# Optimization experiments

Measured on AMD Instinct MI355X. Metric: run time of the kernel, lower is better.

Reference implementation:

```python
import jax, jax.numpy as jnp
import numpy as np

EMBED = 256
HEADS = 8
LEVELS = 4
POINTS = 4
HD = EMBED // HEADS  # 32
SHAPES = np.array([[100, 100], [50, 50], [25, 25], [13, 13]], dtype=np.int64)  # (H_l, W_l)


def setup_inputs() -> dict:
    key = jax.random.key(0)
    ks = jax.random.split(key, 12)
    nv = int(SHAPES.prod(-1).sum())  # 13294
    bs, nq, d = 2, nv, EMBED
    level_start = np.concatenate([[0], SHAPES.prod(-1).cumsum()[:-1]])
    s = 0.02
    return {
        "query": jax.random.normal(ks[0], (bs, nq, d), jnp.float32),
        "reference_points": jax.random.uniform(ks[1], (bs, nq, LEVELS, 2), jnp.float32),
        "value": jax.random.normal(ks[2], (bs, nv, d), jnp.float32),
        "spatial_shapes": jnp.asarray(SHAPES, jnp.int32),
        "level_start_index": jnp.asarray(level_start, jnp.int32),
        "key_padding_mask": jnp.zeros((bs, nv), jnp.bool_),
        "W_samp": jax.random.normal(ks[3], (HEADS * LEVELS * POINTS * 2, d), jnp.float32) * s,
        "b_samp": jax.random.normal(ks[4], (HEADS * LEVELS * POINTS * 2,), jnp.float32),
        "W_attn": jax.random.normal(ks[5], (HEADS * LEVELS * POINTS, d), jnp.float32) * s,
        "b_attn": jnp.zeros((HEADS * LEVELS * POINTS,), jnp.float32),
        "W_val": jax.random.normal(ks[6], (d, d), jnp.float32) * s,
        "b_val": jnp.zeros((d,), jnp.float32),
        "W_out": jax.random.normal(ks[7], (d, d), jnp.float32) * s,
        "b_out": jnp.zeros((d,), jnp.float32),
    }


def _msda_core(value_bhnd, shapes_np, starts_np, loc, attn):
    """value_bhnd: (bs, H, nv, hd); loc: (bs, nq, H, L, P, 2) in [0,1]; attn: (bs, nq, H, L, P)."""
    bs, heads, nv, hd = value_bhnd.shape
    nq = loc.shape[1]
    out = jnp.zeros((bs, nq, heads, hd), value_bhnd.dtype)
    for l in range(LEVELS):
        H, W = int(shapes_np[l, 0]), int(shapes_np[l, 1])
        start = int(starts_np[l])
        v = jax.lax.dynamic_slice_in_dim(value_bhnd, start, H * W, axis=2)  # (bs, heads, H*W, hd)
        # grid_sample(align_corners=False): pixel coord = loc * size - 0.5
        lx = loc[:, :, :, l, :, 0] * W - 0.5  # (bs, nq, heads, P)
        ly = loc[:, :, :, l, :, 1] * H - 0.5
        x0 = jnp.floor(lx)
        y0 = jnp.floor(ly)
        tx = lx - x0
        ty = ly - y0
        x0i = x0.astype(jnp.int32)
        y0i = y0.astype(jnp.int32)
        samp = jnp.zeros((bs, heads, nq, POINTS, hd), value_bhnd.dtype)
        for dy, wy in ((0, 1.0 - ty), (1, ty)):
            for dx, wx in ((0, 1.0 - tx), (1, tx)):
                xi = x0i + dx
                yi = y0i + dy
                valid = (xi >= 0) & (xi < W) & (yi >= 0) & (yi < H)  # zeros padding
                idx = jnp.clip(yi, 0, H - 1) * W + jnp.clip(xi, 0, W - 1)  # (bs, nq, heads, P)
                idx_t = idx.transpose(0, 2, 1, 3).reshape(bs, heads, nq * POINTS)
                g = jnp.take_along_axis(v, idx_t[..., None], axis=2)
                g = g.reshape(bs, heads, nq, POINTS, hd)
                w = jnp.where(valid, wx * wy, 0.0).transpose(0, 2, 1, 3)[..., None]
                samp = samp + g * w
        out = out + jnp.einsum("bhqpd,bqhp->bqhd", samp, attn[:, :, :, l, :])
    return out.reshape(bs, nq, heads * hd)


def reference(query, reference_points, value, spatial_shapes, level_start_index,
              key_padding_mask, W_samp, b_samp, W_attn, b_attn, W_val, b_val, W_out, b_out):
    bs, nq, d = query.shape
    v = value @ W_val.T + b_val
    v = jnp.where(key_padding_mask[..., None], 0.0, v)
    v = v.reshape(bs, -1, HEADS, HD).transpose(0, 2, 1, 3)  # (bs, heads, nv, hd)
    off = (query @ W_samp.T + b_samp).reshape(bs, nq, HEADS, LEVELS, POINTS, 2)
    attn = (query @ W_attn.T + b_attn).reshape(bs, nq, HEADS, LEVELS * POINTS)
    attn = jax.nn.softmax(attn, axis=-1).reshape(bs, nq, HEADS, LEVELS, POINTS)
    ss = np.asarray(spatial_shapes)
    starts = np.asarray(level_start_index)
    # offset normalizer is (W, H) per level
    norm = jnp.asarray(ss[:, ::-1].copy(), jnp.float32)
    loc = reference_points[:, :, None, :, None, :] + off / norm[None, None, None, :, None, :]
    out = _msda_core(v, ss, starts, loc, attn)
    return out @ W_out.T + b_out
```

## Files before the change

kernel.cpp:

```cpp
#include <hip/hip_runtime.h>
#include <hip/hip_bf16.h>
#include <hip/hip_fp16.h>
#include <cstdint>
#include <cstddef>

#define EMBED  256
#define NV_PER_B 13294
#define M_PAD   26624
#define NQPB   8

__constant__ const int c_H[4]  = {100, 50, 25, 13};
__constant__ const int c_W[4]  = {100, 50, 25, 13};
__constant__ const int c_ST[4] = {0, 10000, 12500, 13125};

typedef __attribute__((ext_vector_type(8))) short bf16x8;
typedef __attribute__((ext_vector_type(4))) float f32x4;

__device__ inline short f2bf(float x) {
    __hip_bfloat16 h = __float2bfloat16(x);
    return *reinterpret_cast<short*>(&h);
}

__global__ __launch_bounds__(256) void convert_kernel(
    const float* __restrict__ q,  const float* __restrict__ v,
    const float* __restrict__ wv, const float* __restrict__ wsamp,
    const float* __restrict__ wattn, const float* __restrict__ wo,
    const float* __restrict__ bsamp, const float* __restrict__ battn,
    short* __restrict__ q_bf, short* __restrict__ v_bf,
    short* __restrict__ wv_bf, short* __restrict__ wcat_bf,
    short* __restrict__ wo_bf, float* __restrict__ bias_cat,
    int n_real4, int n_pad4)
{
    const int i = blockIdx.x * 256 + threadIdx.x;
    if (i < n_pad4) {
        float4 a = make_float4(0.f, 0.f, 0.f, 0.f);
        float4 b = make_float4(0.f, 0.f, 0.f, 0.f);
        if (i < n_real4) {
            a = ((const float4*)q)[i];
            b = ((const float4*)v)[i];
        }
        ((short4*)q_bf)[i] = make_short4(f2bf(a.x), f2bf(a.y), f2bf(a.z), f2bf(a.w));
        ((short4*)v_bf)[i] = make_short4(f2bf(b.x), f2bf(b.y), f2bf(b.z), f2bf(b.w));
    }
    if (i < 16384) {
        float4 a = ((const float4*)wv)[i];
        float4 c = ((const float4*)wo)[i];
        ((short4*)wv_bf)[i] = make_short4(f2bf(a.x), f2bf(a.y), f2bf(a.z), f2bf(a.w));
        ((short4*)wo_bf)[i] = make_short4(f2bf(c.x), f2bf(c.y), f2bf(c.z), f2bf(c.w));
    }
    if (i < 24576) {
        float4 a = (i < 16384) ? ((const float4*)wsamp)[i]
                               : ((const float4*)wattn)[i - 16384];
        ((short4*)wcat_bf)[i] = make_short4(f2bf(a.x), f2bf(a.y), f2bf(a.z), f2bf(a.w));
    }
    if (i < 96) {
        float4 a = (i < 64) ? ((const float4*)bsamp)[i]
                            : ((const float4*)battn)[i - 64];
        ((float4*)bias_cat)[i] = a;
    }
}

__device__ __forceinline__ void gemm_kloop(
    const short* __restrict__ A, const short* __restrict__ Wt,
    int bm, int bn, char* smem, f32x4 (&acc)[4][4],
    int t, int wave, int lane)
{
    constexpr int K = 256;
    const int row0 = t >> 2, row1 = row0 + 64;
    const int kbl  = t & 3;
    const int kbg0 = kbl ^ (row0 & 3);
    const int kbg1 = kbl ^ (row1 & 3);
    const size_t a0 = (size_t)(bm + row0) * K + kbg0 * 8;
    const size_t a1 = (size_t)(bm + row1) * K + kbg1 * 8;
    const size_t b0 = (size_t)(bn + row0) * K + kbg0 * 8;
    const size_t b1 = (size_t)(bn + row1) * K + kbg1 * 8;
    const int lr16 = lane & 15, qk = lane >> 4;
    const int swz  = (qk ^ (lr16 & 3)) * 16;
    const int wrow = wave & 1, wcol = wave >> 1;

    auto issue = [&](int stage, int k0) {
        char* sa = smem + stage * 16384 + wave * 1024;
        char* sb = sa + 8192;
        __builtin_amdgcn_global_load_lds(
            (const __attribute__((address_space(1))) void*)(A + a0 + k0),
            (__attribute__((address_space(3))) void*)(sa), 16, 0, 0);
        __builtin_amdgcn_global_load_lds(
            (const __attribute__((address_space(1))) void*)(A + a1 + k0),
            (__attribute__((address_space(3))) void*)(sa + 4096), 16, 0, 0);
        __builtin_amdgcn_global_load_lds(
            (const __attribute__((address_space(1))) void*)(Wt + b0 + k0),
            (__attribute__((address_space(3))) void*)(sb), 16, 0, 0);
        __builtin_amdgcn_global_load_lds(
            (const __attribute__((address_space(1))) void*)(Wt + b1 + k0),
            (__attribute__((address_space(3))) void*)(sb + 4096), 16, 0, 0);
    };

    issue(0, 0);
    #pragma unroll
    for (int it = 0; it < 8; ++it) {
        __syncthreads();
        if (it + 1 < 8) issue((it + 1) & 1, (it + 1) * 32);
        const char* sa = smem + (it & 1) * 16384;
        const char* sb = sa + 8192;
        bf16x8 af[4], bfr[4];
        #pragma unroll
        for (int mi = 0; mi < 4; ++mi)
            af[mi] = *(const bf16x8*)(sa + (wrow * 64 + mi * 16 + lr16) * 64 + swz);
        #pragma unroll
        for (int ni = 0; ni < 4; ++ni)
            bfr[ni] = *(const bf16x8*)(sb + (wcol * 64 + ni * 16 + lr16) * 64 + swz);
        #pragma unroll
        for (int mi = 0; mi < 4; ++mi)
            #pragma unroll
            for (int ni = 0; ni < 4; ++ni)
                acc[mi][ni] = __builtin_amdgcn_mfma_f32_16x16x32_bf16(
                    af[mi], bfr[ni], acc[mi][ni], 0, 0, 0);
    }
}

__global__ __launch_bounds__(256) void gemm_mega_kernel(
    const short* __restrict__ v_bf, const short* __restrict__ wv_bf,
    const float* __restrict__ b_val, __half* __restrict__ vproj,
    const short* __restrict__ q_bf, const short* __restrict__ wcat_bf,
    const float* __restrict__ bias_cat, __half* __restrict__ qo)
{
    __shared__ __align__(16) char smem[36864];
    const int t = threadIdx.x;
    const int wave = t >> 6, lane = t & 63;
    const int lr16 = lane & 15, qk = lane >> 4;
    const int wrow = wave & 1, wcol = wave >> 1;
    const int y = blockIdx.y;
    const int bm = blockIdx.x * 128;

    const short* A; const short* Wt; const float* bias; __half* Cc; int Nst, bn;
    if (y < 2) { A = v_bf; Wt = wv_bf;   bias = b_val;    Cc = vproj; Nst = 256; bn = y * 128; }
    else       { A = q_bf; Wt = wcat_bf; bias = bias_cat; Cc = qo;    Nst = 384; bn = (y - 2) * 128; }

    f32x4 acc[4][4] = {};
    gemm_kloop(A, Wt, bm, bn, smem, acc, t, wave, lane);

    __syncthreads();
    __half* ep = (__half*)(smem + wave * 9216);
    const int colbase = bn + wcol * 64;
    float bv[4];
    #pragma unroll
    for (int ni = 0; ni < 4; ++ni) bv[ni] = bias[colbase + ni * 16 + lr16];
    #pragma unroll
    for (int mi = 0; mi < 4; ++mi)
        #pragma unroll
        for (int ni = 0; ni < 4; ++ni)
            #pragma unroll
            for (int r = 0; r < 4; ++r)
                ep[(mi * 16 + qk * 4 + r) * 72 + ni * 16 + lr16] =
                    __float2half(acc[mi][ni][r] + bv[ni]);
    __syncthreads();
    const int er = lane >> 3, ec = (lane & 7) * 8;
    #pragma unroll
    for (int pass = 0; pass < 8; ++pass) {
        const int r = pass * 8 + er;
        const int4 vv = *(const int4*)&ep[r * 72 + ec];
        const int grow = bm + wrow * 64 + r;
        *(int4*)&Cc[(size_t)grow * Nst + colbase + ec] = vv;
    }
}

__global__ __launch_bounds__(256) void gemm_out_kernel(
    const short* __restrict__ corebf, const short* __restrict__ wo_bf,
    const float* __restrict__ b_out, float* __restrict__ C, int M)
{
    __shared__ __align__(16) char smem[36864];
    const int t = threadIdx.x;
    const int wave = t >> 6, lane = t & 63;
    const int lr16 = lane & 15, qk = lane >> 4;
    const int wrow = wave & 1, wcol = wave >> 1;
    const int bm = blockIdx.x * 128, bn = blockIdx.y * 128;

    f32x4 acc[4][4] = {};
    gemm_kloop(corebf, wo_bf, bm, bn, smem, acc, t, wave, lane);

    const int colbase = bn + wcol * 64;
    float bv[4];
    #pragma unroll
    for (int ni = 0; ni < 4; ++ni) bv[ni] = b_out[colbase + ni * 16 + lr16];
    float* ep = (float*)(smem + wave * 8704);
    #pragma unroll
    for (int p = 0; p < 2; ++p) {
        __syncthreads();
        #pragma unroll
        for (int mh = 0; mh < 2; ++mh) {
            const int mi = p * 2 + mh;
            #pragma unroll
            for (int ni = 0; ni < 4; ++ni)
                #pragma unroll
                for (int r = 0; r < 4; ++r)
                    ep[(mh * 16 + qk * 4 + r) * 68 + ni * 16 + lr16] =
                        acc[mi][ni][r] + bv[ni];
        }
        __syncthreads();
        const int er = lane >> 4, ec = (lane & 15) * 4;
        #pragma unroll
        for (int j = 0; j < 8; ++j) {
            const int r = j * 4 + er;
            const float4 vv = *(const float4*)&ep[r * 68 + ec];
            const int grow = bm + wrow * 64 + p * 32 + r;
            if (grow < M)
                *(float4*)&C[(size_t)grow * 256 + colbase + ec] = vv;
        }
    }
}

__global__ __launch_bounds__(256) void msda_core_kernel(
    const __half* __restrict__ vproj,
    const float* __restrict__ refp,
    const __half* __restrict__ qo,
    short* __restrict__ core,
    int nq, int nv, int M)
{
    const int bq0 = blockIdx.x * NQPB;
    const int t = threadIdx.x;

    __shared__ float s_w[NQPB * 128];
    __shared__ float s_ref[NQPB * 8];
    __shared__ unsigned int s_tap[NQPB * 8][65];

    #pragma unroll
    for (int i = 0; i < 4; ++i) {
        const int s = t + i * 256;
        const int q = s >> 7, r = s & 127;
        s_w[s] = __half2float(qo[(size_t)(bq0 + q) * 384 + 256 + r]);
    }
    if (t < NQPB * 8) {
        const int gq = min(bq0 + (t >> 3), M - 1);
        s_ref[t] = refp[(size_t)gq * 8 + (t & 7)];
    }
    __syncthreads();

    if (t < NQPB * 8) {
        const int base = (t >> 3) * 128 + (t & 7) * 16;
        float m = -1e30f;
        #pragma unroll
        for (int j = 0; j < 16; ++j) m = fmaxf(m, s_w[base + j]);
        float e[16]; float ssum = 0.f;
        #pragma unroll
        for (int j = 0; j < 16; ++j) { e[j] = expf(s_w[base + j] - m); ssum += e[j]; }
        const float inv = 1.f / ssum;
        #pragma unroll
        for (int j = 0; j < 16; ++j) s_w[base + j] = e[j] * inv;
    }
    __syncthreads();

    #pragma unroll
    for (int i = 0; i < 4; ++i) {
        const int s = t + i * 256;
        const int q = s >> 7, r = s & 127;
        const int h = r >> 4, lp = r & 15, l = lp >> 2;
        const int gq = bq0 + q;
        const float2 off = __half22float2(*(const __half2*)&qo[(size_t)gq * 384 + r * 2]);
        const float rx = s_ref[q * 8 + l * 2];
        const float ry = s_ref[q * 8 + l * 2 + 1];
        const int W = c_W[l], H = c_H[l], st = c_ST[l];
        const float fW = (float)W, fH = (float)H;
        const float lx = (rx + off.x / fW) * fW - 0.5f;
        const float ly = (ry + off.y / fH) * fH - 0.5f;
        const float x0f = floorf(lx), y0f = floorf(ly);
        const float fx = lx - x0f, fy = ly - y0f;
        const int x0 = (int)x0f, y0 = (int)y0f;
        const float aw = s_w[s];
        const float wx[2] = {1.f - fx, fx};
        const float wy[2] = {1.f - fy, fy};
        #pragma unroll
        for (int dy = 0; dy < 2; ++dy) {
            #pragma unroll
            for (int dx = 0; dx < 2; ++dx) {
                const int xi = x0 + dx, yi = y0 + dy;
                const bool ok = (xi >= 0) & (xi < W) & (yi >= 0) & (yi < H);
                const unsigned int idx = ok ? (unsigned int)(st + yi * W + xi) : 0u;
                const float w = ok ? aw * wy[dy] * wx[dx] : 0.f;
                const unsigned int pw = (unsigned int)__half_as_ushort(__float2half(w));
                s_tap[q * 8 + h][lp * 4 + dy * 2 + dx] = idx | (pw << 16);
            }
        }
    }
    __syncthreads();

    const int q   = t >> 5;
    const int l32 = t & 31;
    const int h   = l32 >> 2;
    const int c8  = l32 & 3;
    const int gq  = bq0 + q;
    const int b   = (gq >= nq) ? 1 : 0;
    const __half* __restrict__ vb = vproj + (size_t)b * nv * EMBED + h * 32 + c8 * 8;
    const unsigned int* __restrict__ taps = s_tap[q * 8 + h];

    float a[8] = {0.f, 0.f, 0.f, 0.f, 0.f, 0.f, 0.f, 0.f};
    #pragma unroll 8
    for (int j = 0; j < 64; ++j) {
        const unsigned int u = taps[j];
        const float w = __half2float(__ushort_as_half((unsigned short)(u >> 16)));
        const int4 raw = *(const int4*)(vb + (size_t)(u & 0xFFFFu) * EMBED);
        const __half2* hh = (const __half2*)&raw;
        float2 f;
        f = __half22float2(hh[0]); a[0] = fmaf(w, f.x, a[0]); a[1] = fmaf(w, f.y, a[1]);
        f = __half22float2(hh[1]); a[2] = fmaf(w, f.x, a[2]); a[3] = fmaf(w, f.y, a[3]);
        f = __half22float2(hh[2]); a[4] = fmaf(w, f.x, a[4]); a[5] = fmaf(w, f.y, a[5]);
        f = __half22float2(hh[3]); a[6] = fmaf(w, f.x, a[6]); a[7] = fmaf(w, f.y, a[7]);
    }

    if (gq < M) {
        __align__(16) short o[8];
        #pragma unroll
        for (int i = 0; i < 8; ++i) o[i] = f2bf(a[i]);
        *(int4*)&core[(size_t)gq * 256 + h * 32 + c8 * 8] = *(const int4*)o;
    }
}

extern "C" void kernel_launch(void* const* d_in, const int* in_sizes, int n_in,
                              void* d_out, int out_size, void* d_ws, size_t ws_size,
                              hipStream_t stream) {
    const float* query  = (const float*)d_in[0];
    const float* refp   = (const float*)d_in[1];
    const float* value  = (const float*)d_in[2];
    const float* W_samp = (const float*)d_in[6];
    const float* b_samp = (const float*)d_in[7];
    const float* W_attn = (const float*)d_in[8];
    const float* b_attn = (const float*)d_in[9];
    const float* W_val  = (const float*)d_in[10];
    const float* b_val  = (const float*)d_in[11];
    const float* W_out  = (const float*)d_in[12];
    const float* b_out  = (const float*)d_in[13];
    float* out = (float*)d_out;

    const int M  = in_sizes[0] / EMBED;
    const int nq = NV_PER_B;
    const int nv = NV_PER_B;
    const int Mp = M_PAD;

    char* p = (char*)d_ws;
    short*  q_bf   = (short*)p;  p += (size_t)Mp * 256 * 2;
    short*  v_bf   = (short*)p;  p += (size_t)Mp * 256 * 2;
    short*  corebf = (short*)p;  p += (size_t)Mp * 256 * 2;
    __half* vproj  = (__half*)p; p += (size_t)Mp * 256 * 2;
    __half* qo     = (__half*)p; p += (size_t)Mp * 384 * 2;
    short*  wv_bf  = (short*)p;  p += 65536 * 2;
    short*  wcat   = (short*)p;  p += 98304 * 2;
    short*  wo_bf  = (short*)p;  p += 65536 * 2;
    float*  biascat= (float*)p;  p += 384 * 4;

    const int n_real4 = M * 256 / 4;
    const int n_pad4  = Mp * 256 / 4;
    dim3 blk(256);

    convert_kernel<<<dim3((n_pad4 + 255) / 256), blk, 0, stream>>>(
        query, value, W_val, W_samp, W_attn, W_out, b_samp, b_attn,
        q_bf, v_bf, wv_bf, wcat, wo_bf, biascat, n_real4, n_pad4);

    const int mb = Mp / 128;
    gemm_mega_kernel<<<dim3(mb, 5), blk, 0, stream>>>(
        v_bf, wv_bf, b_val, vproj, q_bf, wcat, biascat, qo);

    msda_core_kernel<<<dim3((M + NQPB - 1) / NQPB), blk, 0, stream>>>(
        vproj, refp, qo, corebf, nq, nv, M);

    gemm_out_kernel<<<dim3(mb, 2), blk, 0, stream>>>(
        corebf, wo_bf, b_out, out, M);
}
```

Before: 206.1 us.

## Store value projection head-major and gather adjacent x-taps as one 64-byte row

The value-projection GEMM epilogue now writes vproj in a per-batch, per-head layout (b, head, nv, 32), so the two horizontally adjacent bilinear taps become one contiguous 128-byte span. The sampling kernel clamps x0 so each tap pair is read from that span, with the x weights folded into the clamped pair. It now handles 2 queries per block, with 8 lanes per (head, row) and a shuffle reduction across rows and channel groups. Softmax moves to warp shuffles, removing shared-memory staging and two barriers. The gains should come from better gather coalescing and less block-level setup, at the cost of more shuffles and a scattered epilogue write.

```diff
diff --git a/kernel.cpp b/kernel.cpp
--- a/kernel.cpp
+++ b/kernel.cpp
@@ -7,7 +7,7 @@
 #define EMBED  256
 #define NV_PER_B 13294
 #define M_PAD   26624
-#define NQPB   8
+#define QPB    2
 
 __constant__ const int c_H[4]  = {100, 50, 25, 13};
 __constant__ const int c_W[4]  = {100, 50, 25, 13};
@@ -160,7 +160,18 @@
         const int r = pass * 8 + er;
         const int4 vv = *(const int4*)&ep[r * 72 + ec];
         const int grow = bm + wrow * 64 + r;
-        *(int4*)&Cc[(size_t)grow * Nst + colbase + ec] = vv;
+        if (y < 2) {
+            if (grow < 2 * NV_PER_B) {
+                const int bb  = (grow >= NV_PER_B) ? 1 : 0;
+                const int ii  = grow - bb * NV_PER_B;
+                const int col = colbase + ec;
+                const size_t dst =
+                    ((size_t)(bb * 8 + (col >> 5)) * NV_PER_B + ii) * 32 + (col & 31);
+                *(int4*)&Cc[dst] = vv;
+            }
+        } else {
+            *(int4*)&Cc[(size_t)grow * Nst + colbase + ec] = vv;
+        }
     }
 }
 
@@ -216,48 +227,29 @@
     short* __restrict__ core,
     int nq, int nv, int M)
 {
-    const int bq0 = blockIdx.x * NQPB;
     const int t = threadIdx.x;
-
-    __shared__ float s_w[NQPB * 128];
-    __shared__ float s_ref[NQPB * 8];
-    __shared__ unsigned int s_tap[NQPB * 8][65];
-
-    #pragma unroll
-    for (int i = 0; i < 4; ++i) {
-        const int s = t + i * 256;
-        const int q = s >> 7, r = s & 127;
-        s_w[s] = __half2float(qo[(size_t)(bq0 + q) * 384 + 256 + r]);
-    }
-    if (t < NQPB * 8) {
-        const int gq = min(bq0 + (t >> 3), M - 1);
-        s_ref[t] = refp[(size_t)gq * 8 + (t & 7)];
-    }
-    __syncthreads();
-
-    if (t < NQPB * 8) {
-        const int base = (t >> 3) * 128 + (t & 7) * 16;
-        float m = -1e30f;
-        #pragma unroll
-        for (int j = 0; j < 16; ++j) m = fmaxf(m, s_w[base + j]);
-        float e[16]; float ssum = 0.f;
-        #pragma unroll
-        for (int j = 0; j < 16; ++j) { e[j] = expf(s_w[base + j] - m); ssum += e[j]; }
-        const float inv = 1.f / ssum;
-        #pragma unroll
-        for (int j = 0; j < 16; ++j) s_w[base + j] = e[j] * inv;
-    }
-    __syncthreads();
-
-    #pragma unroll
-    for (int i = 0; i < 4; ++i) {
-        const int s = t + i * 256;
-        const int q = s >> 7, r = s & 127;
+    const int q = t >> 7;
+    const int r = t & 127;
+    const int gq = blockIdx.x * QPB + q;
+
+    __shared__ uint2 s_tap[QPB][8][2][17];
+
+    {
         const int h = r >> 4, lp = r & 15, l = lp >> 2;
-        const int gq = bq0 + q;
+        const int gqc = min(gq, M - 1);
+        const float logit = __half2float(qo[(size_t)gq * 384 + 256 + r]);
+        float m = logit;
+        #pragma unroll
+        for (int s = 1; s < 16; s <<= 1) m = fmaxf(m, __shfl_xor(m, s));
+        const float ev = expf(logit - m);
+        float ssum = ev;
+        #pragma unroll
+        for (int s = 1; s < 16; s <<= 1) ssum += __shfl_xor(ssum, s);
+        const float aw = ev / ssum;
+
         const float2 off = __half22float2(*(const __half2*)&qo[(size_t)gq * 384 + r * 2]);
-        const float rx = s_ref[q * 8 + l * 2];
-        const float ry = s_ref[q * 8 + l * 2 + 1];
+        const float rx = refp[(size_t)gqc * 8 + l * 2];
+        const float ry = refp[(size_t)gqc * 8 + l * 2 + 1];
         const int W = c_W[l], H = c_H[l], st = c_ST[l];
         const float fW = (float)W, fH = (float)H;
         const float lx = (rx + off.x / fW) * fW - 0.5f;
@@ -265,39 +257,40 @@
         const float x0f = floorf(lx), y0f = floorf(ly);
         const float fx = lx - x0f, fy = ly - y0f;
         const int x0 = (int)x0f, y0 = (int)y0f;
-        const float aw = s_w[s];
-        const float wx[2] = {1.f - fx, fx};
-        const float wy[2] = {1.f - fy, fy};
+        const int x0c = min(max(x0, 0), W - 2);
+        const float wx0 = (x0c == x0) ? (1.f - fx) : ((x0c == x0 + 1) ? fx : 0.f);
+        const float wx1 = (x0c + 1 == x0) ? (1.f - fx) : ((x0c == x0) ? fx : 0.f);
         #pragma unroll
         for (int dy = 0; dy < 2; ++dy) {
-            #pragma unroll
-            for (int dx = 0; dx < 2; ++dx) {
-                const int xi = x0 + dx, yi = y0 + dy;
-                const bool ok = (xi >= 0) & (xi < W) & (yi >= 0) & (yi < H);
-                const unsigned int idx = ok ? (unsigned int)(st + yi * W + xi) : 0u;
-                const float w = ok ? aw * wy[dy] * wx[dx] : 0.f;
-                const unsigned int pw = (unsigned int)__half_as_ushort(__float2half(w));
-                s_tap[q * 8 + h][lp * 4 + dy * 2 + dx] = idx | (pw << 16);
-            }
+            const int yv = y0 + dy;
+            const bool okY = (yv >= 0) & (yv < H);
+            const int yc = min(max(yv, 0), H - 1);
+            const float wy = okY ? (dy ? fy : (1.f - fy)) * aw : 0.f;
+            const unsigned int boff = (unsigned int)((st + yc * W + x0c) << 6);
+            const unsigned int pw =
+                (unsigned int)__half_as_ushort(__float2half(wy * wx0)) |
+                ((unsigned int)__half_as_ushort(__float2half(wy * wx1)) << 16);
+            s_tap[q][h][dy][lp] = make_uint2(boff, pw);
         }
     }
     __syncthreads();
 
-    const int q   = t >> 5;
-    const int l32 = t & 31;
-    const int h   = l32 >> 2;
-    const int c8  = l32 & 3;
-    const int gq  = bq0 + q;
+    const int h   = r >> 4;
+    const int y   = (r >> 3) & 1;
+    const int e   = r & 7;
+    const int wsh = (e & 4) << 2;
+    const int c8  = e & 3;
     const int b   = (gq >= nq) ? 1 : 0;
-    const __half* __restrict__ vb = vproj + (size_t)b * nv * EMBED + h * 32 + c8 * 8;
-    const unsigned int* __restrict__ taps = s_tap[q * 8 + h];
-
+    const char* __restrict__ vb =
+        (const char*)(vproj + ((size_t)(b * 8 + h) * (size_t)nv) * 32) + e * 16;
+
+    const uint2* taps = s_tap[q][h][y];
     float a[8] = {0.f, 0.f, 0.f, 0.f, 0.f, 0.f, 0.f, 0.f};
     #pragma unroll 8
-    for (int j = 0; j < 64; ++j) {
-        const unsigned int u = taps[j];
-        const float w = __half2float(__ushort_as_half((unsigned short)(u >> 16)));
-        const int4 raw = *(const int4*)(vb + (size_t)(u & 0xFFFFu) * EMBED);
+    for (int p = 0; p < 16; ++p) {
+        const uint2 tp = taps[p];
+        const float w = __half2float(__ushort_as_half((unsigned short)(tp.y >> wsh)));
+        const int4 raw = *(const int4*)(vb + tp.x);
         const __half2* hh = (const __half2*)&raw;
         float2 f;
         f = __half22float2(hh[0]); a[0] = fmaf(w, f.x, a[0]); a[1] = fmaf(w, f.y, a[1]);
@@ -305,8 +298,12 @@
         f = __half22float2(hh[2]); a[4] = fmaf(w, f.x, a[4]); a[5] = fmaf(w, f.y, a[5]);
         f = __half22float2(hh[3]); a[6] = fmaf(w, f.x, a[6]); a[7] = fmaf(w, f.y, a[7]);
     }
-
-    if (gq < M) {
+    #pragma unroll
+    for (int i = 0; i < 8; ++i) a[i] += __shfl_xor(a[i], 4);
+    #pragma unroll
+    for (int i = 0; i < 8; ++i) a[i] += __shfl_xor(a[i], 8);
+
+    if (((r & 12) == 0) && gq < M) {
         __align__(16) short o[8];
         #pragma unroll
         for (int i = 0; i < 8; ++i) o[i] = f2bf(a[i]);
@@ -358,7 +355,7 @@
     gemm_mega_kernel<<<dim3(mb, 5), blk, 0, stream>>>(
         v_bf, wv_bf, b_val, vproj, q_bf, wcat, biascat, qo);
 
-    msda_core_kernel<<<dim3((M + NQPB - 1) / NQPB), blk, 0, stream>>>(
+    msda_core_kernel<<<dim3((M + QPB - 1) / QPB), blk, 0, stream>>>(
         vproj, refp, qo, corebf, nq, nv, M);
 
     gemm_out_kernel<<<dim3(mb, 2), blk, 0, stream>>>(
```

New measurement: 206.6 us. Within noise of the previous version (+0.3%).
